# Kernel optimization log

Measured on AMD Instinct MI355X. Metric: run time of the kernel, lower is better.

Reference implementation:

```python
import jax, jax.numpy as jnp
import numpy as np

B, T, F, H, C = 32, 512, 512, 1024, 1000


def setup_inputs() -> dict:
    key = jax.random.key(0)
    ks = jax.random.split(key, 9)
    return {
        "data": jax.random.normal(ks[0], (B, T, F), dtype=jnp.float32),
        "h0": jax.random.normal(ks[1], (H,), dtype=jnp.float32),
        "c0": jax.random.normal(ks[2], (H,), dtype=jnp.float32),
        "w_f": jax.random.normal(ks[3], (H + F, H), dtype=jnp.float32),
        "w_i": jax.random.normal(ks[4], (H + F, H), dtype=jnp.float32),
        "w_c1": jax.random.normal(ks[5], (H + F, H), dtype=jnp.float32),
        "w_o": jax.random.normal(ks[6], (H + F, H), dtype=jnp.float32),
        "fc_w": jax.random.normal(ks[7], (C, H), dtype=jnp.float32),
        "fc_b": jax.random.normal(ks[8], (C,), dtype=jnp.float32),
    }


def reference(data, h0, c0, w_f, w_i, w_c1, w_o, fc_w, fc_b):
    b, t, _ = data.shape
    h = h0.shape[0]
    # Original module never updates h0/c0 inside the time loop, so every
    # timestep sees the same initial state; vectorize gates over time.
    z = jnp.concatenate([jnp.broadcast_to(h0, (b, t, h)), data], axis=-1)  # [B,T,H+F]
    # Stack the 4 gate weights into one fused matmul: [H+F, 4H]
    w_all = jnp.concatenate([w_f, w_i, w_c1, w_o], axis=1)
    g = jnp.einsum('btz,zk->btk', z, w_all)  # [B,T,4H]
    f_g, i_g, c1_g, o_g = jnp.split(g, 4, axis=-1)
    f_g = jax.nn.sigmoid(f_g)
    i_g = jax.nn.sigmoid(i_g)
    c1_g = jnp.tanh(c1_g)
    o_g = jax.nn.sigmoid(o_g)
    c = f_g * c0 + i_g * c1_g          # [B,T,H]
    h_all = o_g * jnp.tanh(c)          # [B,T,H]
    h_last = h_all[:, -1]              # output depends on last timestep only
    logits = jax.nn.relu(h_last @ fc_w.T + fc_b)
    return jax.nn.log_softmax(logits, axis=1)
```

## Files before the change

kernel.cpp:

```cpp
#include <hip/hip_runtime.h>
#include <math.h>

#define BB 32
#define TT 512
#define FF 512
#define HH 1024
#define CC 1000
#define QQ (4*HH)
#define FCB 8

template<int JCH, int CHH, int JCD, int CHD>
__global__ __launch_bounds__(512, 4) void k_gates(
    const float* __restrict__ data, const float* __restrict__ h0,
    const float* __restrict__ wf, const float* __restrict__ wi,
    const float* __restrict__ wc, const float* __restrict__ wo,
    float* __restrict__ hp, float* __restrict__ dp)
{
    constexpr int LDSN = (BB*JCD > JCH) ? BB*JCD : JCH;
    __shared__ float lds[LDSN];
    const int t  = threadIdx.x;
    const int bx = blockIdx.x;
    constexpr int NH0 = 2*CHH;

    if (bx < NH0) {
        const int cb2 = bx & 1;
        const int ch  = bx >> 1;
        const int q   = cb2*2048 + t*4;
        const int gate = q >> 10;
        const int k4   = q & (HH-1);
        const float* w = (gate==0) ? wf : (gate==1) ? wi : (gate==2) ? wc : wo;
        if (t < JCH) lds[t] = h0[ch*JCH + t];
        __syncthreads();
        float4 s = make_float4(0.f,0.f,0.f,0.f);
        #pragma unroll
        for (int j = 0; j < JCH; j += 4) {
            const float4 w0 = *(const float4*)(w + (size_t)(ch*JCH + j+0)*HH + k4);
            const float4 w1 = *(const float4*)(w + (size_t)(ch*JCH + j+1)*HH + k4);
            const float4 w2 = *(const float4*)(w + (size_t)(ch*JCH + j+2)*HH + k4);
            const float4 w3 = *(const float4*)(w + (size_t)(ch*JCH + j+3)*HH + k4);
            const float h0v = lds[j+0], h1v = lds[j+1], h2v = lds[j+2], h3v = lds[j+3];
            s.x += h0v*w0.x; s.y += h0v*w0.y; s.z += h0v*w0.z; s.w += h0v*w0.w;
            s.x += h1v*w1.x; s.y += h1v*w1.y; s.z += h1v*w1.z; s.w += h1v*w1.w;
            s.x += h2v*w2.x; s.y += h2v*w2.y; s.z += h2v*w2.z; s.w += h2v*w2.w;
            s.x += h3v*w3.x; s.y += h3v*w3.y; s.z += h3v*w3.z; s.w += h3v*w3.w;
        }
        *(float4*)(hp + (size_t)ch*QQ + q) = s;
    } else {
        const int idx  = bx - NH0;
        const int cb   = idx & 15;
        const int cd   = idx >> 4;
        const int q0   = cb*256;
        const int gate = q0 >> 10;
        const int k0   = q0 & (HH-1);
        const float* w = (gate==0) ? wf : (gate==1) ? wi : (gate==2) ? wc : wo;
        const int jc0  = cd*JCD;

        constexpr int SL = BB*JCD/4;
        for (int s = t; s < SL; s += 512) {
            const int b  = s / (JCD/4);
            const int jj = (s % (JCD/4))*4;
            const float4 v = *(const float4*)(data + (size_t)b*TT*FF + (size_t)(TT-1)*FF + jc0 + jj);
            lds[b*JCD + jj+0] = v.x; lds[b*JCD + jj+1] = v.y;
            lds[b*JCD + jj+2] = v.z; lds[b*JCD + jj+3] = v.w;
        }
        __syncthreads();

        const int c4 = t & 63;
        const int b0 = (t >> 6) * 4;
        const int k4 = k0 + c4*4;
        float4 acc[4];
        #pragma unroll
        for (int bi = 0; bi < 4; ++bi) acc[bi] = make_float4(0.f,0.f,0.f,0.f);

        #pragma unroll 2
        for (int j = 0; j < JCD; j += 4) {
            const float4 w0 = *(const float4*)(w + (size_t)(HH + jc0 + j+0)*HH + k4);
            const float4 w1 = *(const float4*)(w + (size_t)(HH + jc0 + j+1)*HH + k4);
            const float4 w2 = *(const float4*)(w + (size_t)(HH + jc0 + j+2)*HH + k4);
            const float4 w3 = *(const float4*)(w + (size_t)(HH + jc0 + j+3)*HH + k4);
            #pragma unroll
            for (int bi = 0; bi < 4; ++bi) {
                const float d0 = lds[(b0+bi)*JCD + j+0];
                const float d1 = lds[(b0+bi)*JCD + j+1];
                const float d2 = lds[(b0+bi)*JCD + j+2];
                const float d3 = lds[(b0+bi)*JCD + j+3];
                acc[bi].x += d0*w0.x; acc[bi].y += d0*w0.y; acc[bi].z += d0*w0.z; acc[bi].w += d0*w0.w;
                acc[bi].x += d1*w1.x; acc[bi].y += d1*w1.y; acc[bi].z += d1*w1.z; acc[bi].w += d1*w1.w;
                acc[bi].x += d2*w2.x; acc[bi].y += d2*w2.y; acc[bi].z += d2*w2.z; acc[bi].w += d2*w2.w;
                acc[bi].x += d3*w3.x; acc[bi].y += d3*w3.y; acc[bi].z += d3*w3.z; acc[bi].w += d3*w3.w;
            }
        }
        #pragma unroll
        for (int bi = 0; bi < 4; ++bi)
            *(float4*)(dp + ((size_t)cd*BB + b0 + bi)*QQ + q0 + c4*4) = acc[bi];
    }
}

template<int CH, int CD>
__global__ __launch_bounds__(256, 2) void k_cell(
    const float* __restrict__ hp, const float* __restrict__ dp,
    const float* __restrict__ c0, float* __restrict__ hlast)
{
    __shared__ float4 p[4][64];
    const int t    = threadIdx.x;
    const int kblk = blockIdx.x;
    const int b    = blockIdx.y;
    const int g    = t >> 6;
    const int i    = t & 63;
    const int q    = g*HH + kblk*256 + i*4;

    float4 s = make_float4(0.f,0.f,0.f,0.f);
    #pragma unroll 8
    for (int ch = 0; ch < CH; ++ch) {
        const float4 v = *(const float4*)(hp + (size_t)ch*QQ + q);
        s.x += v.x; s.y += v.y; s.z += v.z; s.w += v.w;
    }
    #pragma unroll 8
    for (int cd = 0; cd < CD; ++cd) {
        const float4 v = *(const float4*)(dp + ((size_t)cd*BB + b)*QQ + q);
        s.x += v.x; s.y += v.y; s.z += v.z; s.w += v.w;
    }
    p[g][i] = s;
    __syncthreads();

    if (t < 64) {
        const float4 gf = p[0][t], gi = p[1][t], gc = p[2][t], go = p[3][t];
        const float4 cv = *(const float4*)(c0 + kblk*256 + t*4);
        float4 h;
        {
            const float f = 1.f/(1.f + expf(-gf.x)), ii = 1.f/(1.f + expf(-gi.x));
            const float cg = tanhf(gc.x), o = 1.f/(1.f + expf(-go.x));
            h.x = o*tanhf(f*cv.x + ii*cg);
        }
        {
            const float f = 1.f/(1.f + expf(-gf.y)), ii = 1.f/(1.f + expf(-gi.y));
            const float cg = tanhf(gc.y), o = 1.f/(1.f + expf(-go.y));
            h.y = o*tanhf(f*cv.y + ii*cg);
        }
        {
            const float f = 1.f/(1.f + expf(-gf.z)), ii = 1.f/(1.f + expf(-gi.z));
            const float cg = tanhf(gc.z), o = 1.f/(1.f + expf(-go.z));
            h.z = o*tanhf(f*cv.z + ii*cg);
        }
        {
            const float f = 1.f/(1.f + expf(-gf.w)), ii = 1.f/(1.f + expf(-gi.w));
            const float cg = tanhf(gc.w), o = 1.f/(1.f + expf(-go.w));
            h.w = o*tanhf(f*cv.w + ii*cg);
        }
        *(float4*)(hlast + (size_t)b*HH + kblk*256 + t*4) = h;
    }
}

__global__ __launch_bounds__(256) void k_fc_gemm(
    const float* __restrict__ hlast, const float* __restrict__ fcw,
    const float* __restrict__ fcb, float* __restrict__ logits)
{
    __shared__ float hs[BB][260];
    __shared__ float wl[FCB][260];
    const int t  = threadIdx.x;
    const int c0 = blockIdx.x * FCB;
    const int b  = t & 31;
    const int cl = t >> 5;
    const int c  = c0 + cl;
    float acc = 0.f;
    #pragma unroll
    for (int kc = 0; kc < HH/256; ++kc) {
        const int k0 = kc*256;
        for (int l = t; l < BB*64; l += 256) {
            const int bb = l >> 6, kk = l & 63;
            *(float4*)&hs[bb][kk<<2] = *(const float4*)(hlast + (size_t)bb*HH + k0 + (kk<<2));
        }
        for (int l = t; l < FCB*64; l += 256) {
            const int cc = l >> 6, kk = l & 63;
            *(float4*)&wl[cc][kk<<2] = *(const float4*)(fcw + (size_t)(c0+cc)*HH + k0 + (kk<<2));
        }
        __syncthreads();
        #pragma unroll 8
        for (int k4 = 0; k4 < 64; ++k4) {
            const float4 h4 = *(const float4*)&hs[b][k4<<2];
            const float4 w4 = *(const float4*)&wl[cl][k4<<2];
            acc += h4.x*w4.x + h4.y*w4.y + h4.z*w4.z + h4.w*w4.w;
        }
        __syncthreads();
    }
    logits[(size_t)b*CC + c] = fmaxf(acc + fcb[c], 0.f);
}

__global__ __launch_bounds__(256) void k_lsm(float* __restrict__ out)
{
    __shared__ float red[8];
    const int b = blockIdx.x, t = threadIdx.x;
    float v[4]; float vmax = -1e30f;
    #pragma unroll
    for (int ci = 0; ci < 4; ++ci) {
        const int c = t + ci*256;
        v[ci] = (c < CC) ? out[(size_t)b*CC + c] : -1e30f;
        vmax = fmaxf(vmax, v[ci]);
    }
    for (int o = 32; o > 0; o >>= 1) vmax = fmaxf(vmax, __shfl_down(vmax, o, 64));
    const int lane = t & 63, wid = t >> 6;
    if (lane == 0) red[wid] = vmax;
    __syncthreads();
    if (t == 0) red[4] = fmaxf(fmaxf(red[0], red[1]), fmaxf(red[2], red[3]));
    __syncthreads();
    const float m = red[4];
    float se = 0.f;
    #pragma unroll
    for (int ci = 0; ci < 4; ++ci) {
        const int c = t + ci*256;
        if (c < CC) se += expf(v[ci] - m);
    }
    for (int o = 32; o > 0; o >>= 1) se += __shfl_down(se, o, 64);
    if (lane == 0) red[wid] = se;
    __syncthreads();
    if (t == 0) red[5] = m + logf(red[0] + red[1] + red[2] + red[3]);
    __syncthreads();
    const float lse = red[5];
    #pragma unroll
    for (int ci = 0; ci < 4; ++ci) {
        const int c = t + ci*256;
        if (c < CC) out[(size_t)b*CC + c] = v[ci] - lse;
    }
}

extern "C" void kernel_launch(void* const* d_in, const int* in_sizes, int n_in,
                              void* d_out, int out_size, void* d_ws, size_t ws_size,
                              hipStream_t stream) {
    const float* data = (const float*)d_in[0];
    const float* h0   = (const float*)d_in[1];
    const float* c0   = (const float*)d_in[2];
    const float* wf   = (const float*)d_in[3];
    const float* wi   = (const float*)d_in[4];
    const float* wc   = (const float*)d_in[5];
    const float* wo   = (const float*)d_in[6];
    const float* fcw  = (const float*)d_in[7];
    const float* fcb  = (const float*)d_in[8];
    float* out = (float*)d_out;

    const size_t needA = ((size_t)32*QQ + (size_t)16*BB*QQ + (size_t)BB*HH) * 4;
    const bool cfgA = (ws_size >= needA);

    float* ws = (float*)d_ws;
    if (cfgA) {
        float* hp = ws;
        float* dp = hp + (size_t)32*QQ;
        float* hl = dp + (size_t)16*BB*QQ;
        k_gates<32,32,32,16><<<dim3(2*32 + 16*16), 512, 0, stream>>>(data, h0, wf, wi, wc, wo, hp, dp);
        k_cell<32,16><<<dim3(HH/256, BB), 256, 0, stream>>>(hp, dp, c0, hl);
        k_fc_gemm<<<dim3(CC/FCB), 256, 0, stream>>>(hl, fcw, fcb, out);
    } else {
        float* hp = ws;
        float* dp = hp + (size_t)32*QQ;
        float* hl = dp + (size_t)4*BB*QQ;
        k_gates<32,32,128,4><<<dim3(2*32 + 16*4), 512, 0, stream>>>(data, h0, wf, wi, wc, wo, hp, dp);
        k_cell<32,4><<<dim3(HH/256, BB), 256, 0, stream>>>(hp, dp, c0, hl);
        k_fc_gemm<<<dim3(CC/FCB), 256, 0, stream>>>(hl, fcw, fcb, out);
    }
    k_lsm<<<dim3(BB), 256, 0, stream>>>(out);
}
```

Baseline: 38.77 us.

## Split FC GEMM over K into partial sums reduced in log-softmax kernel

The FC layer now runs as a split-K kernel with a 125x4 grid in place of 125 blocks that each loop over all of K. Each block writes partial logits to workspace, and the log-softmax kernel sums the four partials, adds bias and applies relu. The LDS padding also changes from 260 to 257 with scalar stores, to avoid bank conflicts in the scalar inner loop. The aim is more parallelism for a small GEMM on a GPU with many CUs, at the cost of extra workspace traffic and an extra read pass. The fallback path assumes the workspace has room for the partials but does not check for it.

```diff
diff --git a/kernel.cpp b/kernel.cpp
--- a/kernel.cpp
+++ b/kernel.cpp
@@ -8,6 +8,7 @@
 #define CC 1000
 #define QQ (4*HH)
 #define FCB 8
+#define KCN 4
 
 template<int JCH, int CHH, int JCD, int CHD>
 __global__ __launch_bounds__(512, 4) void k_gates(
@@ -151,42 +152,44 @@
     }
 }
 
-__global__ __launch_bounds__(256) void k_fc_gemm(
+__global__ __launch_bounds__(256) void k_fc_part(
     const float* __restrict__ hlast, const float* __restrict__ fcw,
-    const float* __restrict__ fcb, float* __restrict__ logits)
-{
-    __shared__ float hs[BB][260];
-    __shared__ float wl[FCB][260];
+    float* __restrict__ pl)
+{
+    __shared__ float hs[BB][257];
+    __shared__ float wl[FCB][257];
     const int t  = threadIdx.x;
     const int c0 = blockIdx.x * FCB;
+    const int kc = blockIdx.y;
+    const int k0 = kc*256;
     const int b  = t & 31;
     const int cl = t >> 5;
     const int c  = c0 + cl;
+
+    for (int l = t; l < BB*64; l += 256) {
+        const int bb = l >> 6, kk = l & 63;
+        const float4 v = *(const float4*)(hlast + (size_t)bb*HH + k0 + kk*4);
+        hs[bb][kk*4+0] = v.x; hs[bb][kk*4+1] = v.y;
+        hs[bb][kk*4+2] = v.z; hs[bb][kk*4+3] = v.w;
+    }
+    for (int l = t; l < FCB*64; l += 256) {
+        const int cc = l >> 6, kk = l & 63;
+        const float4 v = *(const float4*)(fcw + (size_t)(c0+cc)*HH + k0 + kk*4);
+        wl[cc][kk*4+0] = v.x; wl[cc][kk*4+1] = v.y;
+        wl[cc][kk*4+2] = v.z; wl[cc][kk*4+3] = v.w;
+    }
+    __syncthreads();
+
     float acc = 0.f;
-    #pragma unroll
-    for (int kc = 0; kc < HH/256; ++kc) {
-        const int k0 = kc*256;
-        for (int l = t; l < BB*64; l += 256) {
-            const int bb = l >> 6, kk = l & 63;
-            *(float4*)&hs[bb][kk<<2] = *(const float4*)(hlast + (size_t)bb*HH + k0 + (kk<<2));
-        }
-        for (int l = t; l < FCB*64; l += 256) {
-            const int cc = l >> 6, kk = l & 63;
-            *(float4*)&wl[cc][kk<<2] = *(const float4*)(fcw + (size_t)(c0+cc)*HH + k0 + (kk<<2));
-        }
-        __syncthreads();
-        #pragma unroll 8
-        for (int k4 = 0; k4 < 64; ++k4) {
-            const float4 h4 = *(const float4*)&hs[b][k4<<2];
-            const float4 w4 = *(const float4*)&wl[cl][k4<<2];
-            acc += h4.x*w4.x + h4.y*w4.y + h4.z*w4.z + h4.w*w4.w;
-        }
-        __syncthreads();
-    }
-    logits[(size_t)b*CC + c] = fmaxf(acc + fcb[c], 0.f);
-}
-
-__global__ __launch_bounds__(256) void k_lsm(float* __restrict__ out)
+    #pragma unroll 16
+    for (int k = 0; k < 256; ++k)
+        acc += hs[b][k] * wl[cl][k];
+    pl[((size_t)kc*BB + b)*CC + c] = acc;
+}
+
+__global__ __launch_bounds__(256) void k_lsm(
+    const float* __restrict__ pl, const float* __restrict__ fcb,
+    float* __restrict__ out)
 {
     __shared__ float red[8];
     const int b = blockIdx.x, t = threadIdx.x;
@@ -194,8 +197,15 @@
     #pragma unroll
     for (int ci = 0; ci < 4; ++ci) {
         const int c = t + ci*256;
-        v[ci] = (c < CC) ? out[(size_t)b*CC + c] : -1e30f;
-        vmax = fmaxf(vmax, v[ci]);
+        if (c < CC) {
+            float s = pl[((size_t)0*BB + b)*CC + c]
+                    + pl[((size_t)1*BB + b)*CC + c]
+                    + pl[((size_t)2*BB + b)*CC + c]
+                    + pl[((size_t)3*BB + b)*CC + c]
+                    + fcb[c];
+            v[ci] = fmaxf(s, 0.f);
+            vmax = fmaxf(vmax, v[ci]);
+        } else v[ci] = -1e30f;
     }
     for (int o = 32; o > 0; o >>= 1) vmax = fmaxf(vmax, __shfl_down(vmax, o, 64));
     const int lane = t & 63, wid = t >> 6;
@@ -237,7 +247,7 @@
     const float* fcb  = (const float*)d_in[8];
     float* out = (float*)d_out;
 
-    const size_t needA = ((size_t)32*QQ + (size_t)16*BB*QQ + (size_t)BB*HH) * 4;
+    const size_t needA = ((size_t)32*QQ + (size_t)16*BB*QQ + (size_t)BB*HH + (size_t)KCN*BB*CC) * 4;
     const bool cfgA = (ws_size >= needA);
 
     float* ws = (float*)d_ws;
@@ -245,16 +255,19 @@
         float* hp = ws;
         float* dp = hp + (size_t)32*QQ;
         float* hl = dp + (size_t)16*BB*QQ;
+        float* pl = hl + (size_t)BB*HH;
         k_gates<32,32,32,16><<<dim3(2*32 + 16*16), 512, 0, stream>>>(data, h0, wf, wi, wc, wo, hp, dp);
         k_cell<32,16><<<dim3(HH/256, BB), 256, 0, stream>>>(hp, dp, c0, hl);
-        k_fc_gemm<<<dim3(CC/FCB), 256, 0, stream>>>(hl, fcw, fcb, out);
+        k_fc_part<<<dim3(CC/FCB, KCN), 256, 0, stream>>>(hl, fcw, pl);
+        k_lsm<<<dim3(BB), 256, 0, stream>>>(pl, fcb, out);
     } else {
         float* hp = ws;
         float* dp = hp + (size_t)32*QQ;
         float* hl = dp + (size_t)4*BB*QQ;
+        float* pl = hl + (size_t)BB*HH;
         k_gates<32,32,128,4><<<dim3(2*32 + 16*4), 512, 0, stream>>>(data, h0, wf, wi, wc, wo, hp, dp);
         k_cell<32,4><<<dim3(HH/256, BB), 256, 0, stream>>>(hp, dp, c0, hl);
-        k_fc_gemm<<<dim3(CC/FCB), 256, 0, stream>>>(hl, fcw, fcb, out);
-    }
-    k_lsm<<<dim3(BB), 256, 0, stream>>>(out);
-}
+        k_fc_part<<<dim3(CC/FCB, KCN), 256, 0, stream>>>(hl, fcw, pl);
+        k_lsm<<<dim3(BB), 256, 0, stream>>>(pl, fcb, out);
+    }
+}
```

Result: faster. 31.70 us (-18.2%).
